# Kernel optimization log

Measured on AMD Instinct MI355X. Metric: run time of the kernel, lower is better.

Reference implementation:

```python
import jax, jax.numpy as jnp
import numpy as np

B, N, C = 8, 1025, 768  # batch, tokens (1 CLS + 32*32 patches), channels
H = 12                  # heads
D = C // H              # head dim = 64
EPS = 1e-6

def _rot(x):
    # stack([-x[..., 1::2], x[..., ::2]], -1).reshape(x.shape)
    return jnp.stack([-x[..., 1::2], x[..., ::2]], axis=-1).reshape(x.shape)

def apply_rot_embed_cat(x, emb):
    # emb: [N-1, 2*D] = concat(sin, cos); x: [B, H, N-1, D]
    sin, cos = jnp.split(emb, 2, axis=-1)
    return x * cos + _rot(x) * sin

def setup_inputs() -> dict:
    key = jax.random.key(0)
    ks = jax.random.split(key, 8)
    s = 0.02
    return {
        "x": jax.random.normal(ks[0], (B, N, C), jnp.float32),
        "rope": jax.random.normal(ks[1], (N - 1, 2 * D), jnp.float32),
        "w_qkv": jax.random.normal(ks[2], (C, 3 * C), jnp.float32) * s,
        "q_bias": jax.random.normal(ks[3], (C,), jnp.float32) * s,
        "v_bias": jax.random.normal(ks[4], (C,), jnp.float32) * s,
        "gamma": jnp.ones((C,), jnp.float32),
        "beta": jnp.zeros((C,), jnp.float32),
        "w_proj": jax.random.normal(ks[5], (C, C), jnp.float32) * s,
        "b_proj": jnp.zeros((C,), jnp.float32),
    }

def reference(x, rope, w_qkv, q_bias, v_bias, gamma, beta, w_proj, b_proj):
    scale = D ** (-0.5)
    qkv_bias = jnp.concatenate([q_bias, jnp.zeros_like(q_bias), v_bias], axis=0)
    qkv = x @ w_qkv + qkv_bias  # [B, N, 3C]
    qkv = qkv.reshape(B, N, 3, H, D).transpose(2, 0, 3, 1, 4)  # [3, B, H, N, D]
    q, k, v = qkv[0], qkv[1], qkv[2]
    # RoPE on non-CLS tokens only
    q = jnp.concatenate([q[:, :, :1], apply_rot_embed_cat(q[:, :, 1:], rope)], axis=2)
    k = jnp.concatenate([k[:, :, :1], apply_rot_embed_cat(k[:, :, 1:], rope)], axis=2)
    attn = jnp.einsum('bhqd,bhkd->bhqk', q * scale, k)
    attn = jax.nn.softmax(attn, axis=-1)
    y = jnp.einsum('bhqk,bhkd->bhqd', attn, v)
    y = y.transpose(0, 2, 1, 3).reshape(B, N, C)
    # LayerNorm
    mu = jnp.mean(y, axis=-1, keepdims=True)
    var = jnp.mean(jnp.square(y - mu), axis=-1, keepdims=True)
    y = (y - mu) * jax.lax.rsqrt(var + EPS) * gamma + beta
    return y @ w_proj + b_proj
```

## Files before the change

kernel.cpp:

```cpp
#include <hip/hip_runtime.h>

typedef __bf16 bf16_t;
typedef __bf16 bf16x8 __attribute__((ext_vector_type(8)));
typedef float f32x4 __attribute__((ext_vector_type(4)));
typedef float f32x16 __attribute__((ext_vector_type(16)));
typedef unsigned short u16;
typedef unsigned int u32;

#define NTOK 1025
#define MTOT 8200
#define MPAD 8448
#define CDIM 768

__device__ __forceinline__ u16 f2bf(float f) {
  union { float f; unsigned u; } v; v.f = f;
  unsigned r = v.u + 0x7fffu + ((v.u >> 16) & 1u);
  return (u16)(r >> 16);
}
__device__ __forceinline__ float bf2f(u16 h) {
  union { unsigned u; float f; } v; v.u = ((unsigned)h) << 16; return v.f;
}
__device__ __forceinline__ u32 cvtpk(float lo, float hi) {
  u32 r; asm("v_cvt_pk_bf16_f32 %0, %1, %2" : "=v"(r) : "v"(lo), "v"(hi)); return r;
}
__device__ __forceinline__ void gld16(const void* g, void* l) {
  __builtin_amdgcn_global_load_lds(
      (const __attribute__((address_space(1))) unsigned*)g,
      (__attribute__((address_space(3))) unsigned*)l, 16, 0, 0);
}

__global__ void conv_x(const float4* __restrict__ in, u16* __restrict__ out, int n4) {
  int i = blockIdx.x * blockDim.x + threadIdx.x;
  if (i < n4) {
    float4 f = in[i];
    ushort4 o; o.x = f2bf(f.x); o.y = f2bf(f.y); o.z = f2bf(f.z); o.w = f2bf(f.w);
    *(ushort4*)&out[i * 4] = o;
  }
}

__global__ __launch_bounds__(256) void transp(const float* __restrict__ in,
                                              u16* __restrict__ out, int K, int N) {
  __shared__ float tile[32][33];
  int n0 = blockIdx.x * 32, k0 = blockIdx.y * 32;
  int tx = threadIdx.x & 31, ty = threadIdx.x >> 5;
#pragma unroll
  for (int i = 0; i < 4; ++i)
    tile[ty + i * 8][tx] = in[(k0 + ty + i * 8) * N + n0 + tx];
  __syncthreads();
#pragma unroll
  for (int i = 0; i < 4; ++i)
    out[(n0 + ty + i * 8) * K + k0 + tx] = f2bf(tile[tx][ty + i * 8]);
}

template <bool TRANS>
__device__ __forceinline__ void kloop128(const u16* __restrict__ A, const u16* __restrict__ Bt,
                                         int m0, int n0, u16* As, u16* Bs, int t,
                                         f32x4 (*acc)[4]) {
  const int K = 768;
  int lane = t & 63, wave = t >> 6;
  int ln = lane & 15, hi = lane >> 4;
  int wr = wave >> 1, wc = wave & 1;
  int swz = (ln & 7) << 4;
  int trow = t >> 3;
  int tcolb = (t & 7) * 16;
  int scol = ((tcolb ^ ((trow & 7) << 4)) >> 1);

  for (int k0 = 0; k0 < K; k0 += 64) {
#pragma unroll
    for (int c = 0; c < 4; ++c) {
      gld16(&A[(size_t)(m0 + c * 32 + trow) * K + k0 + scol], &As[c * 2048 + t * 8]);
      gld16(&Bt[(size_t)(n0 + c * 32 + trow) * K + k0 + scol], &Bs[c * 2048 + t * 8]);
    }
    asm volatile("s_waitcnt vmcnt(0)" ::: "memory");
    __builtin_amdgcn_s_barrier();
    asm volatile("" ::: "memory");
#pragma unroll
    for (int kk = 0; kk < 2; ++kk) {
      bf16x8 af[4], bfr[4];
#pragma unroll
      for (int i = 0; i < 4; ++i)
        af[i] = *(const bf16x8*)((const char*)&As[(wr * 64 + i * 16 + ln) * 64]
                                 + ((kk * 64 + hi * 16) ^ swz));
#pragma unroll
      for (int j = 0; j < 4; ++j)
        bfr[j] = *(const bf16x8*)((const char*)&Bs[(wc * 64 + j * 16 + ln) * 64]
                                  + ((kk * 64 + hi * 16) ^ swz));
      __builtin_amdgcn_s_setprio(1);
#pragma unroll
      for (int x = 0; x < 4; ++x)
#pragma unroll
        for (int y = 0; y < 4; ++y)
          acc[x][y] = TRANS
              ? __builtin_amdgcn_mfma_f32_16x16x32_bf16(bfr[x], af[y], acc[x][y], 0, 0, 0)
              : __builtin_amdgcn_mfma_f32_16x16x32_bf16(af[x], bfr[y], acc[x][y], 0, 0, 0);
      __builtin_amdgcn_s_setprio(0);
    }
    asm volatile("" ::: "memory");
    __builtin_amdgcn_s_barrier();
  }
}

__global__ __launch_bounds__(256) void qkv_gemm_t(
    const u16* __restrict__ A, const u16* __restrict__ Bt,
    const float* __restrict__ qbias, const float* __restrict__ rope,
    u16* __restrict__ q, u16* __restrict__ kfr) {
  const int NB = 12;
  __shared__ u16 As[8192], Bs[8192];
  int tau0 = blockIdx.x;
  int xcd = tau0 & 7, pos = tau0 >> 3;
  int tau = (xcd < 4) ? xcd * 98 + pos : 392 + (xcd - 4) * 97 + pos;
  int bx = tau % NB, by = tau / NB;
  int m0 = by * 128, n0 = bx * 128;
  int t = threadIdx.x;
  int lane = t & 63, wave = t >> 6;
  int ln = lane & 15, hi = lane >> 4;
  int wr = wave >> 1, wc = wave & 1;

  f32x4 acc[4][4] = {};
  kloop128<true>(A, Bt, m0, n0, As, Bs, t, acc);

  const float scale = 0.125f * 1.4426950408889634f;
#pragma unroll
  for (int ii = 0; ii < 4; ++ii) {
    int m = m0 + wr * 64 + ii * 16 + ln;
    if (m < MTOT) {
      int b = m / NTOK;
      int n = m - b * NTOK;
      const float* rp = rope + (size_t)(n - 1) * 128;
#pragma unroll
      for (int jj = 0; jj < 4; ++jj) {
        int c4 = n0 + wc * 64 + jj * 16 + hi * 4;
        int part = (c4 >= CDIM) ? 1 : 0;
        int cc = c4 - part * CDIM;
        int h = cc >> 6, d4 = cc & 63;
        float v0 = acc[jj][ii][0], v1 = acc[jj][ii][1];
        float v2 = acc[jj][ii][2], v3 = acc[jj][ii][3];
        if (part == 0) {
          float4 qb = *(const float4*)(qbias + cc);
          v0 += qb.x; v1 += qb.y; v2 += qb.z; v3 += qb.w;
        }
        float o0, o1, o2, o3;
        if (n > 0) {
          float4 sn = *(const float4*)(rp + d4);
          float4 cs = *(const float4*)(rp + 64 + d4);
          o0 = v0 * cs.x - v1 * sn.x;
          o1 = v1 * cs.y + v0 * sn.y;
          o2 = v2 * cs.z - v3 * sn.z;
          o3 = v3 * cs.w + v2 * sn.w;
        } else { o0 = v0; o1 = v1; o2 = v2; o3 = v3; }
        uint2 w;
        if (part == 0) {
          w.x = cvtpk(o0 * scale, o1 * scale); w.y = cvtpk(o2 * scale, o3 * scale);
          *(uint2*)(q + ((size_t)(h * MPAD + m)) * 64 + d4) = w;
        } else {
          w.x = cvtpk(o0, o1); w.y = cvtpk(o2, o3);
          int kt2 = n >> 5, lqn = n & 31;
          int sF = d4 >> 4, h2d = (d4 >> 3) & 1, j0 = d4 & 7;
          u16* dst = kfr + ((((size_t)(h * 8 + b) * 34 + kt2) * 4 + sF) * 64
                            + h2d * 32 + lqn) * 8 + j0;
          *(uint2*)dst = w;
        }
      }
    }
  }
}

__global__ __launch_bounds__(256) void qkv_gemm_v(
    const u16* __restrict__ A, const u16* __restrict__ Bt,
    const float* __restrict__ vbias, u16* __restrict__ vfr) {
  const int NB = 6;
  __shared__ u16 As[8192], Bs[8192];
  int tau0 = blockIdx.x;
  int xcd = tau0 & 7, pos = tau0 >> 3;
  int tau = (xcd < 6) ? xcd * 49 + pos : 294 + (xcd - 6) * 48 + pos;
  int bx = tau % NB, by = tau / NB;
  int m0 = by * 128, n0 = 1536 + bx * 128;
  int t = threadIdx.x;
  int lane = t & 63, wave = t >> 6;
  int ln = lane & 15, hi = lane >> 4;
  int wr = wave >> 1, wc = wave & 1;

  f32x4 acc[4][4] = {};
  kloop128<false>(A, Bt, m0, n0, As, Bs, t, acc);

#pragma unroll
  for (int i = 0; i < 4; ++i) {
    int mrow = m0 + wr * 64 + i * 16 + hi * 4;
#pragma unroll
    for (int j = 0; j < 4; ++j) {
      int cv = n0 - 1536 + wc * 64 + j * 16 + ln;
      int h = cv >> 6, d = cv & 63;
      int hf = d >> 5, lqd = d & 31;
      float vb = vbias[cv];
#pragma unroll
      for (int r = 0; r < 4; ++r) {
        int mr = mrow + r;
        if (mr < MTOT) {
          int b = mr / NTOK;
          int n = mr - b * NTOK;
          size_t idx = ((((size_t)(h * 8 + b) * 17 + (n >> 6)) * 4 + ((n >> 4) & 3)) * 2 + hf) * 512
                     + (size_t)((((n >> 3) & 1) * 32 + lqd) * 8 + (n & 7));
          vfr[idx] = f2bf(acc[i][j][r] + vb);
        }
      }
    }
  }
}

template <bool PF, bool MASK>
__device__ __forceinline__ void flash_iter(
    bf16x8 (&kf)[8], bf16x8 (&kn)[8], int pftile, int it,
    const u16* kfb, const u16* vfb, int h2,
    const bf16x8 (&qf)[4], f32x16 (&acc)[2], float& l) {
  if (PF) {
    const u16* kp2 = kfb + (size_t)pftile * 4096;
#pragma unroll
    for (int c = 0; c < 2; ++c)
#pragma unroll
      for (int s = 0; s < 4; ++s)
        kn[c * 4 + s] = *(const bf16x8*)(kp2 + c * 2048 + s * 512);
  }
  bf16x8 vf[8];
  const u16* vp2 = vfb + (size_t)it * 4096;
#pragma unroll
  for (int hf = 0; hf < 2; ++hf)
#pragma unroll
    for (int s = 0; s < 4; ++s)
      vf[hf * 4 + s] = *(const bf16x8*)(vp2 + (s * 2 + hf) * 512);
  f32x16 sc[2] = {};
  __builtin_amdgcn_s_setprio(1);
#pragma unroll
  for (int c = 0; c < 2; ++c)
#pragma unroll
    for (int s = 0; s < 4; ++s)
      sc[c] = __builtin_amdgcn_mfma_f32_32x32x16_bf16(kf[c * 4 + s], qf[s], sc[c], 0, 0, 0);
  __builtin_amdgcn_s_setprio(0);
#pragma unroll
  for (int c = 0; c < 2; ++c)
#pragma unroll
    for (int r = 0; r < 16; ++r)
      sc[c][r] = __builtin_amdgcn_exp2f(sc[c][r]);
  if (MASK) {
#pragma unroll
    for (int c = 0; c < 2; ++c)
#pragma unroll
      for (int r = 0; r < 16; ++r) {
        int kk = it * 64 + c * 32 + (r & 3) + 8 * (r >> 2) + 4 * h2;
        if (kk >= NTOK) sc[c][r] = 0.f;
      }
  }
  float rs = 0.f;
#pragma unroll
  for (int c = 0; c < 2; ++c)
#pragma unroll
    for (int r = 0; r < 16; ++r) rs += sc[c][r];
  l += rs;
  bf16x8 frag[4];
#pragma unroll
  for (int c = 0; c < 2; ++c) {
    u32 k0 = cvtpk(sc[c][0], sc[c][1]),   k1 = cvtpk(sc[c][2], sc[c][3]);
    u32 k2 = cvtpk(sc[c][4], sc[c][5]),   k3 = cvtpk(sc[c][6], sc[c][7]);
    u32 k4 = cvtpk(sc[c][8], sc[c][9]),   k5 = cvtpk(sc[c][10], sc[c][11]);
    u32 k6 = cvtpk(sc[c][12], sc[c][13]), k7 = cvtpk(sc[c][14], sc[c][15]);
    asm("v_permlane32_swap_b32 %0, %1" : "+v"(k0), "+v"(k2));
    asm("v_permlane32_swap_b32 %0, %1" : "+v"(k1), "+v"(k3));
    asm("v_permlane32_swap_b32 %0, %1" : "+v"(k4), "+v"(k6));
    asm("v_permlane32_swap_b32 %0, %1" : "+v"(k5), "+v"(k7));
    union { u32 u[4]; bf16x8 v; } u0, u1;
    u0.u[0] = k0; u0.u[1] = k1; u0.u[2] = k2; u0.u[3] = k3;
    u1.u[0] = k4; u1.u[1] = k5; u1.u[2] = k6; u1.u[3] = k7;
    frag[c * 2] = u0.v; frag[c * 2 + 1] = u1.v;
  }
  __builtin_amdgcn_s_setprio(1);
#pragma unroll
  for (int hf = 0; hf < 2; ++hf)
#pragma unroll
    for (int s = 0; s < 4; ++s)
      acc[hf] = __builtin_amdgcn_mfma_f32_32x32x16_bf16(vf[hf * 4 + s], frag[s], acc[hf], 0, 0, 0);
  __builtin_amdgcn_s_setprio(0);
}

__global__ __launch_bounds__(256, 2) void flash_attn(
    const u16* __restrict__ q, const u16* __restrict__ kfr,
    const u16* __restrict__ vfr, u16* __restrict__ y) {
  int f = blockIdx.x;
  int xcd = f & 7, idx = f >> 3;
  int bh = xcd * 12 + idx / 9;
  int qt = idx - (idx / 9) * 9;
  int b = bh / 12, h = bh - b * 12;
  int t = threadIdx.x, lane = t & 63, w = t >> 6;
  int lq = lane & 31, h2 = lane >> 5;
  int q0 = qt * 128 + w * 32;
  if (q0 >= NTOK) return;
  int qrow = q0 + lq; if (qrow > NTOK - 1) qrow = NTOK - 1;

  const u16* qp = q + ((size_t)(h * MPAD) + (size_t)b * NTOK + qrow) * 64;
  bf16x8 qf[4];
#pragma unroll
  for (int s = 0; s < 4; ++s)
    qf[s] = *(const bf16x8*)&qp[s * 16 + h2 * 8];

  const u16* kfb = kfr + (size_t)(h * 8 + b) * 34 * 2048 + lane * 8;
  const u16* vfb = vfr + (size_t)(h * 8 + b) * 17 * 4096 + lane * 8;

  f32x16 acc[2] = {};
  float l = 0.f;

  bf16x8 ka[8], kb2[8];
#pragma unroll
  for (int c = 0; c < 2; ++c)
#pragma unroll
    for (int s = 0; s < 4; ++s)
      ka[c * 4 + s] = *(const bf16x8*)(kfb + c * 2048 + s * 512);

#pragma unroll 1
  for (int i2 = 0; i2 < 8; ++i2) {
    flash_iter<true, false>(ka, kb2, 2 * i2 + 1, 2 * i2, kfb, vfb, h2, qf, acc, l);
    flash_iter<true, false>(kb2, ka, 2 * i2 + 2, 2 * i2 + 1, kfb, vfb, h2, qf, acc, l);
  }
  flash_iter<false, true>(ka, kb2, 0, 16, kfb, vfb, h2, qf, acc, l);

  int row = q0 + lq;
  if (row < NTOK) {
    float lt = l + __shfl_xor(l, 32, 64);
    float inv = 1.f / lt;
    u16* yr = y + ((size_t)(b * NTOK + row)) * CDIM + h * 64;
#pragma unroll
    for (int hf = 0; hf < 2; ++hf)
#pragma unroll
      for (int g = 0; g < 4; ++g) {
        int d0 = hf * 32 + 8 * g + 4 * h2;
        ushort4 o;
        o.x = f2bf(acc[hf][g * 4 + 0] * inv);
        o.y = f2bf(acc[hf][g * 4 + 1] * inv);
        o.z = f2bf(acc[hf][g * 4 + 2] * inv);
        o.w = f2bf(acc[hf][g * 4 + 3] * inv);
        *(ushort4*)&yr[d0] = o;
      }
  }
}

__global__ __launch_bounds__(256) void lnorm(const u16* __restrict__ y,
                                             const float* __restrict__ gamma,
                                             const float* __restrict__ beta,
                                             u16* __restrict__ out) {
  int row = blockIdx.x;
  const u16* yr = y + (size_t)row * CDIM;
  int t = threadIdx.x;
  float v[3];
  float s = 0.f, s2 = 0.f;
#pragma unroll
  for (int i = 0; i < 3; ++i) {
    v[i] = bf2f(yr[t + 256 * i]);
    s += v[i]; s2 += v[i] * v[i];
  }
#pragma unroll
  for (int msk = 1; msk < 64; msk <<= 1) {
    s  += __shfl_xor(s, msk, 64);
    s2 += __shfl_xor(s2, msk, 64);
  }
  __shared__ float ws[8];
  int w = t >> 6, lane = t & 63;
  if (lane == 0) { ws[w] = s; ws[4 + w] = s2; }
  __syncthreads();
  s = ws[0] + ws[1] + ws[2] + ws[3];
  s2 = ws[4] + ws[5] + ws[6] + ws[7];
  float mu = s * (1.f / 768.f);
  float var = s2 * (1.f / 768.f) - mu * mu;
  float rstd = rsqrtf(var + 1e-6f);
#pragma unroll
  for (int i = 0; i < 3; ++i) {
    int c = t + 256 * i;
    out[(size_t)row * CDIM + c] = f2bf((v[i] - mu) * rstd * gamma[c] + beta[c]);
  }
}

__global__ __launch_bounds__(256) void proj_gemm(
    const u16* __restrict__ A, const u16* __restrict__ Bt,
    const float* __restrict__ bias, float* __restrict__ out) {
  const int NB = 6;
  __shared__ u16 As[8192], Bs[8192];
  int tau0 = blockIdx.x;
  int xcd = tau0 & 7, pos = tau0 >> 3;
  int tau = (xcd < 6) ? xcd * 49 + pos : 294 + (xcd - 6) * 48 + pos;
  int bx = tau % NB, by = tau / NB;
  int m0 = by * 128, n0 = bx * 128;
  int t = threadIdx.x;
  int lane = t & 63, wave = t >> 6;
  int ln = lane & 15, hi = lane >> 4;
  int wr = wave >> 1, wc = wave & 1;

  f32x4 acc[4][4] = {};
  kloop128<true>(A, Bt, m0, n0, As, Bs, t, acc);

#pragma unroll
  for (int ii = 0; ii < 4; ++ii) {
    int m = m0 + wr * 64 + ii * 16 + ln;
    if (m < MTOT) {
      float* dr = out + (size_t)m * CDIM;
#pragma unroll
      for (int jj = 0; jj < 4; ++jj) {
        int c4 = n0 + wc * 64 + jj * 16 + hi * 4;
        float4 bv = *(const float4*)(bias + c4);
        float4 o;
        o.x = acc[jj][ii][0] + bv.x;
        o.y = acc[jj][ii][1] + bv.y;
        o.z = acc[jj][ii][2] + bv.z;
        o.w = acc[jj][ii][3] + bv.w;
        *(float4*)(dr + c4) = o;
      }
    }
  }
}

extern "C" void kernel_launch(void* const* d_in, const int* in_sizes, int n_in,
                              void* d_out, int out_size, void* d_ws, size_t ws_size,
                              hipStream_t stream) {
  const float* x      = (const float*)d_in[0];
  const float* rope   = (const float*)d_in[1];
  const float* w_qkv  = (const float*)d_in[2];
  const float* q_bias = (const float*)d_in[3];
  const float* v_bias = (const float*)d_in[4];
  const float* gamma  = (const float*)d_in[5];
  const float* beta   = (const float*)d_in[6];
  const float* w_proj = (const float*)d_in[7];
  const float* b_proj = (const float*)d_in[8];
  float* out = (float*)d_out;

  char* ws = (char*)d_ws;
  u16* xb    = (u16*)(ws);
  u16* ybf   = (u16*)(ws);
  u16* wqkvt = (u16*)(ws + 12595200);
  u16* wprjt = (u16*)(ws + 16134144);
  u16* qbuf  = (u16*)(ws + 17313792);
  u16* ylb   = (u16*)(ws + 17313792);
  u16* kfr   = (u16*)(ws + 30289920);
  u16* vfr   = (u16*)(ws + 43659264);

  conv_x<<<(1574400 + 255) / 256, 256, 0, stream>>>((const float4*)x, xb, 1574400);
  transp<<<dim3(2304 / 32, 768 / 32), 256, 0, stream>>>(w_qkv, wqkvt, 768, 2304);
  transp<<<dim3(768 / 32, 768 / 32), 256, 0, stream>>>(w_proj, wprjt, 768, 768);

  qkv_gemm_t<<<dim3(780), 256, 0, stream>>>(xb, wqkvt, q_bias, rope, qbuf, kfr);
  qkv_gemm_v<<<dim3(390), 256, 0, stream>>>(xb, wqkvt, v_bias, vfr);
  flash_attn<<<dim3(864), 256, 0, stream>>>(qbuf, kfr, vfr, ybf);
  lnorm<<<8200, 256, 0, stream>>>(ybf, gamma, beta, ylb);
  proj_gemm<<<dim3(390), 256, 0, stream>>>(ylb, wprjt, b_proj, out);
}
```

Baseline: 164.9 us.

## Pre-swizzle GEMM operands into MFMA fragment layout and load directly to registers

The activation and weight operands are rewritten at conversion time (conv_xf, transp_wf, lnorm output) into a per-16-row, per-32-K MFMA fragment layout. The three GEMMs then drop the LDS staging and barriers and load fragments straight from global memory into registers with double buffering, at two blocks per CU. This removes LDS traffic and the per-K-step syncs, in exchange for no data sharing between waves through LDS, so each wave re-reads its A and B fragments from global memory or L2. It also adds a small layout-transform cost in the prep kernels.

```diff
diff --git a/kernel.cpp b/kernel.cpp
--- a/kernel.cpp
+++ b/kernel.cpp
@@ -23,89 +23,91 @@
 __device__ __forceinline__ u32 cvtpk(float lo, float hi) {
   u32 r; asm("v_cvt_pk_bf16_f32 %0, %1, %2" : "=v"(r) : "v"(lo), "v"(hi)); return r;
 }
-__device__ __forceinline__ void gld16(const void* g, void* l) {
-  __builtin_amdgcn_global_load_lds(
-      (const __attribute__((address_space(1))) unsigned*)g,
-      (__attribute__((address_space(3))) unsigned*)l, 16, 0, 0);
-}
-
-__global__ void conv_x(const float4* __restrict__ in, u16* __restrict__ out, int n4) {
-  int i = blockIdx.x * blockDim.x + threadIdx.x;
-  if (i < n4) {
-    float4 f = in[i];
-    ushort4 o; o.x = f2bf(f.x); o.y = f2bf(f.y); o.z = f2bf(f.z); o.w = f2bf(f.w);
-    *(ushort4*)&out[i * 4] = o;
-  }
-}
-
-__global__ __launch_bounds__(256) void transp(const float* __restrict__ in,
-                                              u16* __restrict__ out, int K, int N) {
-  __shared__ float tile[32][33];
-  int n0 = blockIdx.x * 32, k0 = blockIdx.y * 32;
-  int tx = threadIdx.x & 31, ty = threadIdx.x >> 5;
-#pragma unroll
-  for (int i = 0; i < 4; ++i)
-    tile[ty + i * 8][tx] = in[(k0 + ty + i * 8) * N + n0 + tx];
+
+__global__ __launch_bounds__(256) void conv_xf(const float4* __restrict__ x4,
+                                               u16* __restrict__ xf) {
+  __shared__ u16 tile[16][776];
+  int mt = blockIdx.x;
+  int t = threadIdx.x;
+#pragma unroll
+  for (int it = 0; it < 12; ++it) {
+    int id = it * 256 + t;
+    int r = id / 192, c4 = id % 192;
+    int m = mt * 16 + r;
+    if (m < MTOT) {
+      float4 f = x4[(size_t)m * 192 + c4];
+      ushort4 o; o.x = f2bf(f.x); o.y = f2bf(f.y); o.z = f2bf(f.z); o.w = f2bf(f.w);
+      *(ushort4*)&tile[r][c4 * 4] = o;
+    }
+  }
   __syncthreads();
 #pragma unroll
-  for (int i = 0; i < 4; ++i)
-    out[(n0 + ty + i * 8) * K + k0 + tx] = f2bf(tile[tx][ty + i * 8]);
+  for (int it = 0; it < 6; ++it) {
+    int cid = it * 256 + t;
+    int kt = cid >> 6, lane = cid & 63;
+    uint4 w = *(const uint4*)&tile[lane & 15][kt * 32 + (lane >> 4) * 8];
+    *(uint4*)&xf[(((size_t)mt * 24 + kt) * 64 + lane) * 8] = w;
+  }
+}
+
+__global__ __launch_bounds__(64) void transp_wf(const float* __restrict__ in, int N,
+                                                u16* __restrict__ wf) {
+  __shared__ u16 lds[16][32];
+  int n0 = blockIdx.x * 16, k0 = blockIdx.y * 32;
+  int t = threadIdx.x;
+#pragma unroll
+  for (int it = 0; it < 8; ++it) {
+    int e = it * 64 + t;
+    int kk = e >> 4, nn = e & 15;
+    lds[nn][kk] = f2bf(in[(size_t)(k0 + kk) * N + n0 + nn]);
+  }
+  __syncthreads();
+  uint4 w = *(const uint4*)&lds[t & 15][(t >> 4) * 8];
+  *(uint4*)&wf[((((size_t)(n0 >> 4)) * 24 + (k0 >> 5)) * 64 + t) * 8] = w;
 }
 
 template <bool TRANS>
-__device__ __forceinline__ void kloop128(const u16* __restrict__ A, const u16* __restrict__ Bt,
-                                         int m0, int n0, u16* As, u16* Bs, int t,
-                                         f32x4 (*acc)[4]) {
-  const int K = 768;
-  int lane = t & 63, wave = t >> 6;
-  int ln = lane & 15, hi = lane >> 4;
-  int wr = wave >> 1, wc = wave & 1;
-  int swz = (ln & 7) << 4;
-  int trow = t >> 3;
-  int tcolb = (t & 7) * 16;
-  int scol = ((tcolb ^ ((trow & 7) << 4)) >> 1);
-
-  for (int k0 = 0; k0 < K; k0 += 64) {
-#pragma unroll
-    for (int c = 0; c < 4; ++c) {
-      gld16(&A[(size_t)(m0 + c * 32 + trow) * K + k0 + scol], &As[c * 2048 + t * 8]);
-      gld16(&Bt[(size_t)(n0 + c * 32 + trow) * K + k0 + scol], &Bs[c * 2048 + t * 8]);
-    }
-    asm volatile("s_waitcnt vmcnt(0)" ::: "memory");
-    __builtin_amdgcn_s_barrier();
-    asm volatile("" ::: "memory");
-#pragma unroll
-    for (int kk = 0; kk < 2; ++kk) {
-      bf16x8 af[4], bfr[4];
-#pragma unroll
-      for (int i = 0; i < 4; ++i)
-        af[i] = *(const bf16x8*)((const char*)&As[(wr * 64 + i * 16 + ln) * 64]
-                                 + ((kk * 64 + hi * 16) ^ swz));
-#pragma unroll
-      for (int j = 0; j < 4; ++j)
-        bfr[j] = *(const bf16x8*)((const char*)&Bs[(wc * 64 + j * 16 + ln) * 64]
-                                  + ((kk * 64 + hi * 16) ^ swz));
-      __builtin_amdgcn_s_setprio(1);
-#pragma unroll
-      for (int x = 0; x < 4; ++x)
-#pragma unroll
-        for (int y = 0; y < 4; ++y)
-          acc[x][y] = TRANS
-              ? __builtin_amdgcn_mfma_f32_16x16x32_bf16(bfr[x], af[y], acc[x][y], 0, 0, 0)
-              : __builtin_amdgcn_mfma_f32_16x16x32_bf16(af[x], bfr[y], acc[x][y], 0, 0, 0);
-      __builtin_amdgcn_s_setprio(0);
-    }
-    asm volatile("" ::: "memory");
-    __builtin_amdgcn_s_barrier();
-  }
-}
-
-__global__ __launch_bounds__(256) void qkv_gemm_t(
-    const u16* __restrict__ A, const u16* __restrict__ Bt,
+__device__ __forceinline__ void fdloop(const u16* __restrict__ afr, const u16* __restrict__ bfr,
+                                       int m0, int n0, int lane, int wr, int wc,
+                                       f32x4 (*acc)[4]) {
+  const u16* ab = afr + ((size_t)((m0 >> 4) + wr * 4) * 24 * 64 + lane) * 8;
+  const u16* bb = bfr + ((size_t)((n0 >> 4) + wc * 4) * 24 * 64 + lane) * 8;
+  bf16x8 S0[8], S1[8];
+  auto LOAD = [&](bf16x8 (&S)[8], int kt) {
+#pragma unroll
+    for (int i = 0; i < 4; ++i) S[i]     = *(const bf16x8*)(ab + (size_t)i * 12288 + kt * 512);
+#pragma unroll
+    for (int j = 0; j < 4; ++j) S[4 + j] = *(const bf16x8*)(bb + (size_t)j * 12288 + kt * 512);
+  };
+  auto COMP = [&](bf16x8 (&S)[8]) {
+    __builtin_amdgcn_s_setprio(1);
+#pragma unroll
+    for (int x = 0; x < 4; ++x)
+#pragma unroll
+      for (int y = 0; y < 4; ++y)
+        acc[x][y] = TRANS
+            ? __builtin_amdgcn_mfma_f32_16x16x32_bf16(S[4 + x], S[y], acc[x][y], 0, 0, 0)
+            : __builtin_amdgcn_mfma_f32_16x16x32_bf16(S[x], S[4 + y], acc[x][y], 0, 0, 0);
+    __builtin_amdgcn_s_setprio(0);
+  };
+  LOAD(S0, 0);
+#pragma unroll 1
+  for (int k2 = 0; k2 < 11; ++k2) {
+    LOAD(S1, 2 * k2 + 1);
+    COMP(S0);
+    LOAD(S0, 2 * k2 + 2);
+    COMP(S1);
+  }
+  LOAD(S1, 23);
+  COMP(S0);
+  COMP(S1);
+}
+
+__global__ __launch_bounds__(256, 2) void qkv_gemm_t(
+    const u16* __restrict__ xf, const u16* __restrict__ wf,
     const float* __restrict__ qbias, const float* __restrict__ rope,
     u16* __restrict__ q, u16* __restrict__ kfr) {
   const int NB = 12;
-  __shared__ u16 As[8192], Bs[8192];
   int tau0 = blockIdx.x;
   int xcd = tau0 & 7, pos = tau0 >> 3;
   int tau = (xcd < 4) ? xcd * 98 + pos : 392 + (xcd - 4) * 97 + pos;
@@ -117,7 +119,7 @@
   int wr = wave >> 1, wc = wave & 1;
 
   f32x4 acc[4][4] = {};
-  kloop128<true>(A, Bt, m0, n0, As, Bs, t, acc);
+  fdloop<true>(xf, wf, m0, n0, lane, wr, wc, acc);
 
   const float scale = 0.125f * 1.4426950408889634f;
 #pragma unroll
@@ -165,11 +167,10 @@
   }
 }
 
-__global__ __launch_bounds__(256) void qkv_gemm_v(
-    const u16* __restrict__ A, const u16* __restrict__ Bt,
+__global__ __launch_bounds__(256, 2) void qkv_gemm_v(
+    const u16* __restrict__ xf, const u16* __restrict__ wf,
     const float* __restrict__ vbias, u16* __restrict__ vfr) {
   const int NB = 6;
-  __shared__ u16 As[8192], Bs[8192];
   int tau0 = blockIdx.x;
   int xcd = tau0 & 7, pos = tau0 >> 3;
   int tau = (xcd < 6) ? xcd * 49 + pos : 294 + (xcd - 6) * 48 + pos;
@@ -181,7 +182,7 @@
   int wr = wave >> 1, wc = wave & 1;
 
   f32x4 acc[4][4] = {};
-  kloop128<false>(A, Bt, m0, n0, As, Bs, t, acc);
+  fdloop<false>(xf, wf, m0, n0, lane, wr, wc, acc);
 
 #pragma unroll
   for (int i = 0; i < 4; ++i) {
@@ -343,7 +344,7 @@
 __global__ __launch_bounds__(256) void lnorm(const u16* __restrict__ y,
                                              const float* __restrict__ gamma,
                                              const float* __restrict__ beta,
-                                             u16* __restrict__ out) {
+                                             u16* __restrict__ yf) {
   int row = blockIdx.x;
   const u16* yr = y + (size_t)row * CDIM;
   int t = threadIdx.x;
@@ -368,18 +369,23 @@
   float mu = s * (1.f / 768.f);
   float var = s2 * (1.f / 768.f) - mu * mu;
   float rstd = rsqrtf(var + 1e-6f);
-#pragma unroll
-  for (int i = 0; i < 3; ++i) {
-    int c = t + 256 * i;
-    out[(size_t)row * CDIM + c] = f2bf((v[i] - mu) * rstd * gamma[c] + beta[c]);
-  }
-}
-
-__global__ __launch_bounds__(256) void proj_gemm(
-    const u16* __restrict__ A, const u16* __restrict__ Bt,
+  if (t < 96) {
+    union { uint4 u4; u16 u[8]; } iv, ov;
+    iv.u4 = *(const uint4*)&yr[t * 8];
+    const float* gp = gamma + t * 8;
+    const float* bp = beta + t * 8;
+#pragma unroll
+    for (int j = 0; j < 8; ++j)
+      ov.u[j] = f2bf((bf2f(iv.u[j]) - mu) * rstd * gp[j] + bp[j]);
+    int kt = t >> 2, ln2 = (row & 15) + 16 * (t & 3), mt = row >> 4;
+    *(uint4*)&yf[(((size_t)mt * 24 + kt) * 64 + ln2) * 8] = ov.u4;
+  }
+}
+
+__global__ __launch_bounds__(256, 2) void proj_gemm(
+    const u16* __restrict__ yf, const u16* __restrict__ wf,
     const float* __restrict__ bias, float* __restrict__ out) {
   const int NB = 6;
-  __shared__ u16 As[8192], Bs[8192];
   int tau0 = blockIdx.x;
   int xcd = tau0 & 7, pos = tau0 >> 3;
   int tau = (xcd < 6) ? xcd * 49 + pos : 294 + (xcd - 6) * 48 + pos;
@@ -391,7 +397,7 @@
   int wr = wave >> 1, wc = wave & 1;
 
   f32x4 acc[4][4] = {};
-  kloop128<true>(A, Bt, m0, n0, As, Bs, t, acc);
+  fdloop<true>(yf, wf, m0, n0, lane, wr, wc, acc);
 
 #pragma unroll
   for (int ii = 0; ii < 4; ++ii) {
@@ -428,22 +434,22 @@
   float* out = (float*)d_out;
 
   char* ws = (char*)d_ws;
-  u16* xb    = (u16*)(ws);
-  u16* ybf   = (u16*)(ws);
-  u16* wqkvt = (u16*)(ws + 12595200);
-  u16* wprjt = (u16*)(ws + 16134144);
-  u16* qbuf  = (u16*)(ws + 17313792);
-  u16* ylb   = (u16*)(ws + 17313792);
-  u16* kfr   = (u16*)(ws + 30289920);
-  u16* vfr   = (u16*)(ws + 43659264);
-
-  conv_x<<<(1574400 + 255) / 256, 256, 0, stream>>>((const float4*)x, xb, 1574400);
-  transp<<<dim3(2304 / 32, 768 / 32), 256, 0, stream>>>(w_qkv, wqkvt, 768, 2304);
-  transp<<<dim3(768 / 32, 768 / 32), 256, 0, stream>>>(w_proj, wprjt, 768, 768);
-
-  qkv_gemm_t<<<dim3(780), 256, 0, stream>>>(xb, wqkvt, q_bias, rope, qbuf, kfr);
-  qkv_gemm_v<<<dim3(390), 256, 0, stream>>>(xb, wqkvt, v_bias, vfr);
+  u16* xf   = (u16*)(ws);
+  u16* ybf  = (u16*)(ws);
+  u16* wfq  = (u16*)(ws + 12976128);
+  u16* wfp  = (u16*)(ws + 16515072);
+  u16* qbuf = (u16*)(ws + 17694720);
+  u16* yf   = (u16*)(ws + 17694720);
+  u16* kfr  = (u16*)(ws + 30670848);
+  u16* vfr  = (u16*)(ws + 44040192);
+
+  conv_xf<<<dim3(513), 256, 0, stream>>>((const float4*)x, xf);
+  transp_wf<<<dim3(144, 24), 64, 0, stream>>>(w_qkv, 2304, wfq);
+  transp_wf<<<dim3(48, 24), 64, 0, stream>>>(w_proj, 768, wfp);
+
+  qkv_gemm_t<<<dim3(780), 256, 0, stream>>>(xf, wfq, q_bias, rope, qbuf, kfr);
+  qkv_gemm_v<<<dim3(390), 256, 0, stream>>>(xf, wfq, v_bias, vfr);
   flash_attn<<<dim3(864), 256, 0, stream>>>(qbuf, kfr, vfr, ybf);
-  lnorm<<<8200, 256, 0, stream>>>(ybf, gamma, beta, ylb);
-  proj_gemm<<<dim3(390), 256, 0, stream>>>(ylb, wprjt, b_proj, out);
-}
+  lnorm<<<8200, 256, 0, stream>>>(ybf, gamma, beta, yf);
+  proj_gemm<<<dim3(390), 256, 0, stream>>>(yf, wfp, b_proj, out);
+}
```

Result: no change. 167.2 us (+1.4%).

## Use 256x256 GEMM tiles, merge QKV launches, prefetch V in flash loop

Applied to the files above, without the earlier changes.

Replaces the 128x128 GEMM tile loop with a 256x256 tile using 512 threads (8 waves each computing 64x128), merges the separate QK and V projection kernels into one launch with fewer, larger blocks, and enlarges the projection GEMM the same way. In the attention kernel, V fragments are now double-buffered and prefetched one tile ahead alongside K. The goal is more data reuse per LDS load and fewer launches, at the cost of far fewer blocks (297 and 99 on a many-CU GPU), higher register pressure, and larger workspace padding.

```diff
diff --git a/kernel.cpp b/kernel.cpp
--- a/kernel.cpp
+++ b/kernel.cpp
@@ -45,54 +45,61 @@
   int tx = threadIdx.x & 31, ty = threadIdx.x >> 5;
 #pragma unroll
   for (int i = 0; i < 4; ++i)
-    tile[ty + i * 8][tx] = in[(k0 + ty + i * 8) * N + n0 + tx];
+    tile[ty + i * 8][tx] = in[(size_t)(k0 + ty + i * 8) * N + n0 + tx];
   __syncthreads();
 #pragma unroll
   for (int i = 0; i < 4; ++i)
-    out[(n0 + ty + i * 8) * K + k0 + tx] = f2bf(tile[tx][ty + i * 8]);
+    out[(size_t)(n0 + ty + i * 8) * K + k0 + tx] = f2bf(tile[tx][ty + i * 8]);
 }
 
 template <bool TRANS>
-__device__ __forceinline__ void kloop128(const u16* __restrict__ A, const u16* __restrict__ Bt,
+__device__ __forceinline__ void kloop256(const u16* __restrict__ A, const u16* __restrict__ Bt,
                                          int m0, int n0, u16* As, u16* Bs, int t,
-                                         f32x4 (*acc)[4]) {
+                                         f32x4* acc) {
   const int K = 768;
-  int lane = t & 63, wave = t >> 6;
+  int lane = t & 63;
   int ln = lane & 15, hi = lane >> 4;
+  int wave = t >> 6;
   int wr = wave >> 1, wc = wave & 1;
   int swz = (ln & 7) << 4;
-  int trow = t >> 3;
-  int tcolb = (t & 7) * 16;
-  int scol = ((tcolb ^ ((trow & 7) << 4)) >> 1);
 
   for (int k0 = 0; k0 < K; k0 += 64) {
 #pragma unroll
-    for (int c = 0; c < 4; ++c) {
-      gld16(&A[(size_t)(m0 + c * 32 + trow) * K + k0 + scol], &As[c * 2048 + t * 8]);
-      gld16(&Bt[(size_t)(n0 + c * 32 + trow) * K + k0 + scol], &Bs[c * 2048 + t * 8]);
+    for (int l = 0; l < 4; ++l) {
+      int c = t + l * 512;
+      int row = c >> 3, cc = c & 7;
+      int scol = (cc ^ (row & 7)) * 8;
+      gld16(&A[(size_t)(m0 + row) * K + k0 + scol], &As[(size_t)c * 8]);
+      gld16(&Bt[(size_t)(n0 + row) * K + k0 + scol], &Bs[(size_t)c * 8]);
     }
     asm volatile("s_waitcnt vmcnt(0)" ::: "memory");
     __builtin_amdgcn_s_barrier();
     asm volatile("" ::: "memory");
 #pragma unroll
     for (int kk = 0; kk < 2; ++kk) {
-      bf16x8 af[4], bfr[4];
+      bf16x8 af[4], bf[8];
 #pragma unroll
       for (int i = 0; i < 4; ++i)
         af[i] = *(const bf16x8*)((const char*)&As[(wr * 64 + i * 16 + ln) * 64]
                                  + ((kk * 64 + hi * 16) ^ swz));
 #pragma unroll
-      for (int j = 0; j < 4; ++j)
-        bfr[j] = *(const bf16x8*)((const char*)&Bs[(wc * 64 + j * 16 + ln) * 64]
-                                  + ((kk * 64 + hi * 16) ^ swz));
+      for (int j = 0; j < 8; ++j)
+        bf[j] = *(const bf16x8*)((const char*)&Bs[(wc * 128 + j * 16 + ln) * 64]
+                                 + ((kk * 64 + hi * 16) ^ swz));
       __builtin_amdgcn_s_setprio(1);
-#pragma unroll
-      for (int x = 0; x < 4; ++x)
-#pragma unroll
-        for (int y = 0; y < 4; ++y)
-          acc[x][y] = TRANS
-              ? __builtin_amdgcn_mfma_f32_16x16x32_bf16(bfr[x], af[y], acc[x][y], 0, 0, 0)
-              : __builtin_amdgcn_mfma_f32_16x16x32_bf16(af[x], bfr[y], acc[x][y], 0, 0, 0);
+      if (TRANS) {
+#pragma unroll
+        for (int j = 0; j < 8; ++j)
+#pragma unroll
+          for (int i = 0; i < 4; ++i)
+            acc[j * 4 + i] = __builtin_amdgcn_mfma_f32_16x16x32_bf16(bf[j], af[i], acc[j * 4 + i], 0, 0, 0);
+      } else {
+#pragma unroll
+        for (int i = 0; i < 4; ++i)
+#pragma unroll
+          for (int j = 0; j < 8; ++j)
+            acc[i * 8 + j] = __builtin_amdgcn_mfma_f32_16x16x32_bf16(af[i], bf[j], acc[i * 8 + j], 0, 0, 0);
+      }
       __builtin_amdgcn_s_setprio(0);
     }
     asm volatile("" ::: "memory");
@@ -100,107 +107,94 @@
   }
 }
 
-__global__ __launch_bounds__(256) void qkv_gemm_t(
-    const u16* __restrict__ A, const u16* __restrict__ Bt,
-    const float* __restrict__ qbias, const float* __restrict__ rope,
-    u16* __restrict__ q, u16* __restrict__ kfr) {
-  const int NB = 12;
-  __shared__ u16 As[8192], Bs[8192];
+__global__ __launch_bounds__(512, 2) void qkv_gemm_all(
+    const u16* __restrict__ xb, const u16* __restrict__ wqkvt,
+    const float* __restrict__ qbias, const float* __restrict__ vbias,
+    const float* __restrict__ rope,
+    u16* __restrict__ q, u16* __restrict__ kfr, u16* __restrict__ vfr) {
+  __shared__ u16 As[256 * 64], Bs[256 * 64];
+  const int NBX = 9;
   int tau0 = blockIdx.x;
   int xcd = tau0 & 7, pos = tau0 >> 3;
-  int tau = (xcd < 4) ? xcd * 98 + pos : 392 + (xcd - 4) * 97 + pos;
-  int bx = tau % NB, by = tau / NB;
-  int m0 = by * 128, n0 = bx * 128;
+  int tau = (xcd < 1) ? pos : 38 + (xcd - 1) * 37 + pos;
+  int bx = tau % NBX, by = tau / NBX;
+  int m0 = by * 256;
   int t = threadIdx.x;
   int lane = t & 63, wave = t >> 6;
   int ln = lane & 15, hi = lane >> 4;
   int wr = wave >> 1, wc = wave & 1;
 
-  f32x4 acc[4][4] = {};
-  kloop128<true>(A, Bt, m0, n0, As, Bs, t, acc);
-
-  const float scale = 0.125f * 1.4426950408889634f;
-#pragma unroll
-  for (int ii = 0; ii < 4; ++ii) {
-    int m = m0 + wr * 64 + ii * 16 + ln;
-    if (m < MTOT) {
-      int b = m / NTOK;
-      int n = m - b * NTOK;
-      const float* rp = rope + (size_t)(n - 1) * 128;
-#pragma unroll
-      for (int jj = 0; jj < 4; ++jj) {
-        int c4 = n0 + wc * 64 + jj * 16 + hi * 4;
-        int part = (c4 >= CDIM) ? 1 : 0;
-        int cc = c4 - part * CDIM;
-        int h = cc >> 6, d4 = cc & 63;
-        float v0 = acc[jj][ii][0], v1 = acc[jj][ii][1];
-        float v2 = acc[jj][ii][2], v3 = acc[jj][ii][3];
-        if (part == 0) {
-          float4 qb = *(const float4*)(qbias + cc);
-          v0 += qb.x; v1 += qb.y; v2 += qb.z; v3 += qb.w;
+  f32x4 acc[32] = {};
+  int n0 = (bx < 6) ? bx * 256 : 1536 + (bx - 6) * 256;
+  if (bx < 6) kloop256<true>(xb, wqkvt, m0, n0, As, Bs, t, acc);
+  else        kloop256<false>(xb, wqkvt, m0, n0, As, Bs, t, acc);
+
+  if (bx < 6) {
+    const float scale = 0.125f * 1.4426950408889634f;
+#pragma unroll
+    for (int ii = 0; ii < 4; ++ii) {
+      int m = m0 + wr * 64 + ii * 16 + ln;
+      if (m < MTOT) {
+        int b = m / NTOK;
+        int n = m - b * NTOK;
+        const float* rp = rope + (size_t)(n - 1) * 128;
+#pragma unroll
+        for (int jj = 0; jj < 8; ++jj) {
+          int c4 = n0 + wc * 128 + jj * 16 + hi * 4;
+          int part = (c4 >= CDIM) ? 1 : 0;
+          int cc = c4 - part * CDIM;
+          int h = cc >> 6, d4 = cc & 63;
+          f32x4 a = acc[jj * 4 + ii];
+          float v0 = a[0], v1 = a[1], v2 = a[2], v3 = a[3];
+          if (part == 0) {
+            float4 qb = *(const float4*)(qbias + cc);
+            v0 += qb.x; v1 += qb.y; v2 += qb.z; v3 += qb.w;
+          }
+          float o0, o1, o2, o3;
+          if (n > 0) {
+            float4 sn = *(const float4*)(rp + d4);
+            float4 cs = *(const float4*)(rp + 64 + d4);
+            o0 = v0 * cs.x - v1 * sn.x;
+            o1 = v1 * cs.y + v0 * sn.y;
+            o2 = v2 * cs.z - v3 * sn.z;
+            o3 = v3 * cs.w + v2 * sn.w;
+          } else { o0 = v0; o1 = v1; o2 = v2; o3 = v3; }
+          uint2 w;
+          if (part == 0) {
+            w.x = cvtpk(o0 * scale, o1 * scale); w.y = cvtpk(o2 * scale, o3 * scale);
+            *(uint2*)(q + ((size_t)(h * MPAD + m)) * 64 + d4) = w;
+          } else {
+            w.x = cvtpk(o0, o1); w.y = cvtpk(o2, o3);
+            int kt2 = n >> 5, lqn = n & 31;
+            int sF = d4 >> 4, h2d = (d4 >> 3) & 1, j0 = d4 & 7;
+            u16* dst = kfr + ((((size_t)(h * 8 + b) * 34 + kt2) * 4 + sF) * 64
+                              + h2d * 32 + lqn) * 8 + j0;
+            *(uint2*)dst = w;
+          }
         }
-        float o0, o1, o2, o3;
-        if (n > 0) {
-          float4 sn = *(const float4*)(rp + d4);
-          float4 cs = *(const float4*)(rp + 64 + d4);
-          o0 = v0 * cs.x - v1 * sn.x;
-          o1 = v1 * cs.y + v0 * sn.y;
-          o2 = v2 * cs.z - v3 * sn.z;
-          o3 = v3 * cs.w + v2 * sn.w;
-        } else { o0 = v0; o1 = v1; o2 = v2; o3 = v3; }
-        uint2 w;
-        if (part == 0) {
-          w.x = cvtpk(o0 * scale, o1 * scale); w.y = cvtpk(o2 * scale, o3 * scale);
-          *(uint2*)(q + ((size_t)(h * MPAD + m)) * 64 + d4) = w;
-        } else {
-          w.x = cvtpk(o0, o1); w.y = cvtpk(o2, o3);
-          int kt2 = n >> 5, lqn = n & 31;
-          int sF = d4 >> 4, h2d = (d4 >> 3) & 1, j0 = d4 & 7;
-          u16* dst = kfr + ((((size_t)(h * 8 + b) * 34 + kt2) * 4 + sF) * 64
-                            + h2d * 32 + lqn) * 8 + j0;
-          *(uint2*)dst = w;
-        }
       }
     }
-  }
-}
-
-__global__ __launch_bounds__(256) void qkv_gemm_v(
-    const u16* __restrict__ A, const u16* __restrict__ Bt,
-    const float* __restrict__ vbias, u16* __restrict__ vfr) {
-  const int NB = 6;
-  __shared__ u16 As[8192], Bs[8192];
-  int tau0 = blockIdx.x;
-  int xcd = tau0 & 7, pos = tau0 >> 3;
-  int tau = (xcd < 6) ? xcd * 49 + pos : 294 + (xcd - 6) * 48 + pos;
-  int bx = tau % NB, by = tau / NB;
-  int m0 = by * 128, n0 = 1536 + bx * 128;
-  int t = threadIdx.x;
-  int lane = t & 63, wave = t >> 6;
-  int ln = lane & 15, hi = lane >> 4;
-  int wr = wave >> 1, wc = wave & 1;
-
-  f32x4 acc[4][4] = {};
-  kloop128<false>(A, Bt, m0, n0, As, Bs, t, acc);
-
-#pragma unroll
-  for (int i = 0; i < 4; ++i) {
-    int mrow = m0 + wr * 64 + i * 16 + hi * 4;
-#pragma unroll
-    for (int j = 0; j < 4; ++j) {
-      int cv = n0 - 1536 + wc * 64 + j * 16 + ln;
-      int h = cv >> 6, d = cv & 63;
-      int hf = d >> 5, lqd = d & 31;
-      float vb = vbias[cv];
-#pragma unroll
-      for (int r = 0; r < 4; ++r) {
-        int mr = mrow + r;
-        if (mr < MTOT) {
-          int b = mr / NTOK;
-          int n = mr - b * NTOK;
-          size_t idx = ((((size_t)(h * 8 + b) * 17 + (n >> 6)) * 4 + ((n >> 4) & 3)) * 2 + hf) * 512
-                     + (size_t)((((n >> 3) & 1) * 32 + lqd) * 8 + (n & 7));
-          vfr[idx] = f2bf(acc[i][j][r] + vb);
+  } else {
+#pragma unroll
+    for (int i = 0; i < 4; ++i) {
+      int mrow = m0 + wr * 64 + i * 16 + hi * 4;
+#pragma unroll
+      for (int j = 0; j < 8; ++j) {
+        int cv = n0 - 1536 + wc * 128 + j * 16 + ln;
+        int h = cv >> 6, d = cv & 63;
+        int hf = d >> 5, lqd = d & 31;
+        float vb = vbias[cv];
+        f32x4 a = acc[i * 8 + j];
+#pragma unroll
+        for (int r = 0; r < 4; ++r) {
+          int mr = mrow + r;
+          if (mr < MTOT) {
+            int b = mr / NTOK;
+            int n = mr - b * NTOK;
+            size_t idx = ((((size_t)(h * 8 + b) * 17 + (n >> 6)) * 4 + ((n >> 4) & 3)) * 2 + hf) * 512
+                       + (size_t)((((n >> 3) & 1) * 32 + lqd) * 8 + (n & 7));
+            vfr[idx] = f2bf(a[r] + vb);
+          }
         }
       }
     }
@@ -209,7 +203,9 @@
 
 template <bool PF, bool MASK>
 __device__ __forceinline__ void flash_iter(
-    bf16x8 (&kf)[8], bf16x8 (&kn)[8], int pftile, int it,
+    bf16x8 (&kf)[8], bf16x8 (&kn)[8],
+    bf16x8 (&vf)[8], bf16x8 (&vn)[8],
+    int pftile, int it,
     const u16* kfb, const u16* vfb, int h2,
     const bf16x8 (&qf)[4], f32x16 (&acc)[2], float& l) {
   if (PF) {
@@ -219,14 +215,13 @@
 #pragma unroll
       for (int s = 0; s < 4; ++s)
         kn[c * 4 + s] = *(const bf16x8*)(kp2 + c * 2048 + s * 512);
-  }
-  bf16x8 vf[8];
-  const u16* vp2 = vfb + (size_t)it * 4096;
-#pragma unroll
-  for (int hf = 0; hf < 2; ++hf)
-#pragma unroll
-    for (int s = 0; s < 4; ++s)
-      vf[hf * 4 + s] = *(const bf16x8*)(vp2 + (s * 2 + hf) * 512);
+    const u16* vp2 = vfb + (size_t)pftile * 4096;
+#pragma unroll
+    for (int hf = 0; hf < 2; ++hf)
+#pragma unroll
+      for (int s = 0; s < 4; ++s)
+        vn[hf * 4 + s] = *(const bf16x8*)(vp2 + (s * 2 + hf) * 512);
+  }
   f32x16 sc[2] = {};
   __builtin_amdgcn_s_setprio(1);
 #pragma unroll
@@ -306,19 +301,24 @@
   f32x16 acc[2] = {};
   float l = 0.f;
 
-  bf16x8 ka[8], kb2[8];
+  bf16x8 ka[8], kb2[8], va[8], vb[8];
 #pragma unroll
   for (int c = 0; c < 2; ++c)
 #pragma unroll
     for (int s = 0; s < 4; ++s)
       ka[c * 4 + s] = *(const bf16x8*)(kfb + c * 2048 + s * 512);
+#pragma unroll
+  for (int hf = 0; hf < 2; ++hf)
+#pragma unroll
+    for (int s = 0; s < 4; ++s)
+      va[hf * 4 + s] = *(const bf16x8*)(vfb + (s * 2 + hf) * 512);
 
 #pragma unroll 1
   for (int i2 = 0; i2 < 8; ++i2) {
-    flash_iter<true, false>(ka, kb2, 2 * i2 + 1, 2 * i2, kfb, vfb, h2, qf, acc, l);
-    flash_iter<true, false>(kb2, ka, 2 * i2 + 2, 2 * i2 + 1, kfb, vfb, h2, qf, acc, l);
-  }
-  flash_iter<false, true>(ka, kb2, 0, 16, kfb, vfb, h2, qf, acc, l);
+    flash_iter<true, false>(ka, kb2, va, vb, 2 * i2 + 1, 2 * i2, kfb, vfb, h2, qf, acc, l);
+    flash_iter<true, false>(kb2, ka, vb, va, 2 * i2 + 2, 2 * i2 + 1, kfb, vfb, h2, qf, acc, l);
+  }
+  flash_iter<false, true>(ka, kb2, va, vb, 0, 16, kfb, vfb, h2, qf, acc, l);
 
   int row = q0 + lq;
   if (row < NTOK) {
@@ -375,23 +375,23 @@
   }
 }
 
-__global__ __launch_bounds__(256) void proj_gemm(
-    const u16* __restrict__ A, const u16* __restrict__ Bt,
+__global__ __launch_bounds__(512, 2) void proj_gemm(
+    const u16* __restrict__ ylb, const u16* __restrict__ wprjt,
     const float* __restrict__ bias, float* __restrict__ out) {
-  const int NB = 6;
-  __shared__ u16 As[8192], Bs[8192];
+  __shared__ u16 As[256 * 64], Bs[256 * 64];
+  const int NBX = 3;
   int tau0 = blockIdx.x;
   int xcd = tau0 & 7, pos = tau0 >> 3;
-  int tau = (xcd < 6) ? xcd * 49 + pos : 294 + (xcd - 6) * 48 + pos;
-  int bx = tau % NB, by = tau / NB;
-  int m0 = by * 128, n0 = bx * 128;
+  int tau = (xcd < 3) ? xcd * 13 + pos : 39 + (xcd - 3) * 12 + pos;
+  int bx = tau % NBX, by = tau / NBX;
+  int m0 = by * 256, n0 = bx * 256;
   int t = threadIdx.x;
   int lane = t & 63, wave = t >> 6;
   int ln = lane & 15, hi = lane >> 4;
   int wr = wave >> 1, wc = wave & 1;
 
-  f32x4 acc[4][4] = {};
-  kloop128<true>(A, Bt, m0, n0, As, Bs, t, acc);
+  f32x4 acc[32] = {};
+  kloop256<true>(ylb, wprjt, m0, n0, As, Bs, t, acc);
 
 #pragma unroll
   for (int ii = 0; ii < 4; ++ii) {
@@ -399,14 +399,15 @@
     if (m < MTOT) {
       float* dr = out + (size_t)m * CDIM;
 #pragma unroll
-      for (int jj = 0; jj < 4; ++jj) {
-        int c4 = n0 + wc * 64 + jj * 16 + hi * 4;
+      for (int jj = 0; jj < 8; ++jj) {
+        int c4 = n0 + wc * 128 + jj * 16 + hi * 4;
         float4 bv = *(const float4*)(bias + c4);
+        f32x4 a = acc[jj * 4 + ii];
         float4 o;
-        o.x = acc[jj][ii][0] + bv.x;
-        o.y = acc[jj][ii][1] + bv.y;
-        o.z = acc[jj][ii][2] + bv.z;
-        o.w = acc[jj][ii][3] + bv.w;
+        o.x = a[0] + bv.x;
+        o.y = a[1] + bv.y;
+        o.z = a[2] + bv.z;
+        o.w = a[3] + bv.w;
         *(float4*)(dr + c4) = o;
       }
     }
@@ -430,20 +431,20 @@
   char* ws = (char*)d_ws;
   u16* xb    = (u16*)(ws);
   u16* ybf   = (u16*)(ws);
-  u16* wqkvt = (u16*)(ws + 12595200);
-  u16* wprjt = (u16*)(ws + 16134144);
-  u16* qbuf  = (u16*)(ws + 17313792);
-  u16* ylb   = (u16*)(ws + 17313792);
-  u16* kfr   = (u16*)(ws + 30289920);
-  u16* vfr   = (u16*)(ws + 43659264);
-
-  conv_x<<<(1574400 + 255) / 256, 256, 0, stream>>>((const float4*)x, xb, 1574400);
+  u16* wqkvt = (u16*)(ws + 12976128);
+  u16* wprjt = (u16*)(ws + 16515072);
+  u16* qbuf  = (u16*)(ws + 17694720);
+  u16* ylb   = (u16*)(ws + 17694720);
+  u16* kfr   = (u16*)(ws + 30670848);
+  u16* vfr   = (u16*)(ws + 44040192);
+
+  conv_x<<<dim3(6150), 256, 0, stream>>>((const float4*)x, xb, 1574400);
   transp<<<dim3(2304 / 32, 768 / 32), 256, 0, stream>>>(w_qkv, wqkvt, 768, 2304);
   transp<<<dim3(768 / 32, 768 / 32), 256, 0, stream>>>(w_proj, wprjt, 768, 768);
 
-  qkv_gemm_t<<<dim3(780), 256, 0, stream>>>(xb, wqkvt, q_bias, rope, qbuf, kfr);
-  qkv_gemm_v<<<dim3(390), 256, 0, stream>>>(xb, wqkvt, v_bias, vfr);
+  qkv_gemm_all<<<dim3(297), 512, 0, stream>>>(xb, wqkvt, q_bias, v_bias, rope,
+                                              qbuf, kfr, vfr);
   flash_attn<<<dim3(864), 256, 0, stream>>>(qbuf, kfr, vfr, ybf);
   lnorm<<<8200, 256, 0, stream>>>(ybf, gamma, beta, ylb);
-  proj_gemm<<<dim3(390), 256, 0, stream>>>(ylb, wprjt, b_proj, out);
-}
+  proj_gemm<<<dim3(99), 512, 0, stream>>>(ylb, wprjt, b_proj, out);
+}
```

Result: slower. 193.8 us (+17.5%).
